# Performance work log

Hardware: AMD Instinct MI355X
Metric: run time of the kernel (lower is better)

The kernel has to match this reference:

```python
import jax, jax.numpy as jnp
import numpy as np


def setup_inputs() -> dict:
    key = jax.random.key(0)
    kq, kk, kv = jax.random.split(key, 3)
    d_head, sq, skv = 128, 8192, 8192
    q = jax.random.normal(kq, (d_head, sq), dtype=jnp.float32)
    k = jax.random.normal(kk, (d_head, skv), dtype=jnp.float32)
    v = jax.random.normal(kv, (d_head, skv), dtype=jnp.float32)
    return {"q": q, "k": k, "v": v}


def reference(q, k, v):
    # qk: (seqlen_q, seqlen_kv) -- full score matrix, no 1/sqrt(d) scaling (faithful)
    qk = jnp.einsum('dq,dk->qk', q, k)
    row_max = jnp.max(qk, axis=1, keepdims=True)
    exp_row = jnp.exp(qk - row_max)
    scores = exp_row / jnp.sum(exp_row, axis=1, keepdims=True)
    # attn_out: (seqlen_q, d_head)
    attn_out = jnp.einsum('qk,dk->qd', scores, v)
    return attn_out
```

## Files before the change

kernel.cpp:

```cpp
#include <hip/hip_runtime.h>
#include <hip/hip_bf16.h>
#include <math.h>

typedef _Float16 half8 __attribute__((ext_vector_type(8)));
typedef __fp16 fp16x2 __attribute__((ext_vector_type(2)));
typedef float f32x4 __attribute__((ext_vector_type(4)));
typedef float f32x16 __attribute__((ext_vector_type(16)));

#define D 128
#define SQ 8192
#define SKV 8192
#define BQ 256
#define BKV 64
#define LOG2E 1.4426950408889634f
#define DEFER_THR 11.5417f

__device__ __forceinline__ float bf2f(ushort h) {
  union { unsigned u; float f; } v; v.u = ((unsigned)h) << 16;
  return v.f;
}
__device__ __forceinline__ unsigned cvtpk_bf(float a, float b) {
  unsigned r;
  asm("v_cvt_pk_bf16_f32 %0, %1, %2" : "=v"(r) : "v"(a), "v"(b));
  return r;
}
__device__ __forceinline__ unsigned cvtpk_h(float a, float b) {
  union { fp16x2 h; unsigned u; } r;
  r.h = __builtin_amdgcn_cvt_pkrtz(a, b);
  return r.u;
}
__device__ __forceinline__ float fexp2(float x) {
  float r;
  asm("v_exp_f32 %0, %1" : "=v"(r) : "v"(x));
  return r;
}
__device__ __forceinline__ void pl32swap(unsigned& a, unsigned& b) {
  asm("v_permlane32_swap_b32 %0, %1" : "+v"(a), "+v"(b));
}

__global__ void prep_all(const float* __restrict__ q, const float* __restrict__ k,
                         const float* __restrict__ v,
                         _Float16* __restrict__ QT, _Float16* __restrict__ PK,
                         _Float16* __restrict__ PV) {
  int b = blockIdx.x;
  int t = threadIdx.x;
  if (b < 512) {
    const bool isQ = (b < 256);
    const float* src = isQ ? q : k;
    const float scl = isQ ? LOG2E : 1.0f;
    int s0 = (isQ ? b : b - 256) * 32;
    __shared__ float lds[128][33];
    int dr = t >> 5, l = t & 31;
#pragma unroll
    for (int j = 0; j < 16; ++j) {
      int dd = dr * 16 + j;
      lds[dd][l] = src[(size_t)dd * SQ + s0 + l];
    }
    __syncthreads();
#pragma unroll
    for (int i = 0; i < 2; ++i) {
      int cid = t + i * 256;
      int c = cid >> 5, sl = cid & 31;
      half8 hv;
#pragma unroll
      for (int e = 0; e < 8; ++e) hv[e] = (_Float16)(lds[c * 8 + e][sl] * scl);
      if (isQ) {
        *(half8*)(QT + (size_t)(s0 + sl) * D + c * 8) = hv;
      } else {
        int srow = s0 + sl;
        size_t elem = (size_t)((srow >> 5) * 8 + (c >> 1)) * 512 +
                      ((c & 1) * 32 + (srow & 31)) * 8;
        *(half8*)(PK + elem) = hv;
      }
    }
  } else {
    int idx = (b - 512) * 256 + t;
    int i8 = idx * 8;
    float4 x0 = *(const float4*)(v + i8);
    float4 x1 = *(const float4*)(v + i8 + 4);
    int drow = i8 >> 13;
    int kv = i8 & (SKV - 1);
    size_t elem = (size_t)(kv >> 6) * 8192 +
                  (size_t)((drow >> 5) * 4 + ((kv >> 4) & 3)) * 512 +
                  (((kv >> 3) & 1) * 32 + (drow & 31)) * 8;
    half8 hv = { (_Float16)x0.x, (_Float16)x0.y, (_Float16)x0.z, (_Float16)x0.w,
                 (_Float16)x1.x, (_Float16)x1.y, (_Float16)x1.z, (_Float16)x1.w };
    *(half8*)(PV + elem) = hv;
  }
}

__global__ __launch_bounds__(512, 2)
void flash_fwd(const _Float16* __restrict__ QT, const _Float16* __restrict__ PK,
               const _Float16* __restrict__ PV,
               ushort* __restrict__ Opart, float* __restrict__ Mst,
               float* __restrict__ Lst, int splitLen) {
  __shared__ _Float16 Kl[2][BKV * D];
  __shared__ _Float16 Vl[3][BKV * D];

  const int tid = threadIdx.x;
  const int w = tid >> 6;
  const int lane = tid & 63;
  const int lc = lane & 31;
  const int hi = lane >> 5;
  const int qb = blockIdx.x;
  const int split = blockIdx.y;
  const int qrow = qb * BQ + w * 32 + lc;

  half8 qh[8];
#pragma unroll
  for (int ds = 0; ds < 8; ++ds)
    qh[ds] = *(const half8*)(QT + (size_t)qrow * D + ds * 16 + hi * 8);

  f32x16 Ot[4];
#pragma unroll
  for (int dt = 0; dt < 4; ++dt)
#pragma unroll
    for (int e = 0; e < 16; ++e) Ot[dt][e] = 0.f;
  float mrun = -INFINITY, lrun = 0.f;

  const int kvBase = split * splitLen;
  const int nsteps = splitLen / BKV;
  const int tB = kvBase / BKV;

#define STAGE(KB, VB, T)                                                      \
  {                                                                           \
    _Pragma("unroll")                                                         \
    for (int j = 0; j < 4; ++j) {                                             \
      int cblk = w * 4 + j;                                                   \
      int cc = cblk & 15;                                                     \
      const _Float16* gp = ((cblk < 16) ? PK : PV) +                          \
                           (size_t)(T) * (BKV * D) + cc * 512 + lane * 8;     \
      _Float16* lp = ((cblk < 16) ? &Kl[KB][0] : &Vl[VB][0]) + cc * 512;      \
      __builtin_amdgcn_global_load_lds(                                       \
          (const __attribute__((address_space(1))) unsigned*)gp,              \
          (__attribute__((address_space(3))) unsigned*)lp, 16, 0, 0);         \
    }                                                                         \
  }

  auto QKX = [&](int kb2, f32x16& s0, f32x16& s1) {
    const _Float16* kb = &Kl[kb2][0] + lane * 8;
#pragma unroll
    for (int e = 0; e < 16; ++e) { s0[e] = 0.f; s1[e] = 0.f; }
    __builtin_amdgcn_s_setprio(1);
#pragma unroll
    for (int ds = 0; ds < 8; ++ds) {
      half8 k0 = *(const half8*)(kb + ds * 512);
      half8 k1 = *(const half8*)(kb + (8 + ds) * 512);
      s0 = __builtin_amdgcn_mfma_f32_32x32x16_f16(k0, qh[ds], s0, 0, 0, 0);
      s1 = __builtin_amdgcn_mfma_f32_32x32x16_f16(k1, qh[ds], s1, 0, 0, 0);
    }
    __builtin_amdgcn_s_setprio(0);
  };

  auto SMPV = [&](f32x16& s0, f32x16& s1, int vb3) {
    float t8[8];
#pragma unroll
    for (int e = 0; e < 8; ++e)
      t8[e] = fmaxf(fmaxf(s0[e], s0[e + 8]), fmaxf(s1[e], s1[e + 8]));
    float mx = fmaxf(fmaxf(fmaxf(t8[0], t8[4]), fmaxf(t8[1], t8[5])),
                     fmaxf(fmaxf(t8[2], t8[6]), fmaxf(t8[3], t8[7])));
    mx = fmaxf(mx, __shfl_xor(mx, 32));
    if (!__all(mx - mrun <= DEFER_THR)) {
      float mn = fmaxf(mrun, mx);
      float sc = fexp2(mrun - mn);
      mrun = mn;
      lrun *= sc;
#pragma unroll
      for (int dt = 0; dt < 4; ++dt)
#pragma unroll
        for (int e = 0; e < 16; ++e) Ot[dt][e] *= sc;
    }
#pragma unroll
    for (int e = 0; e < 16; ++e) {
      s0[e] = fexp2(s0[e] - mrun);
      s1[e] = fexp2(s1[e] - mrun);
    }
    float a8[8];
#pragma unroll
    for (int e = 0; e < 8; ++e) a8[e] = (s0[e] + s0[e + 8]) + (s1[e] + s1[e + 8]);
    float lsum = ((a8[0] + a8[4]) + (a8[1] + a8[5])) +
                 ((a8[2] + a8[6]) + (a8[3] + a8[7]));
    lsum += __shfl_xor(lsum, 32);
    lrun += lsum;

    unsigned pk[8];
    half8 pb[4];
    union { unsigned u[4]; half8 v; } pbu;
#pragma unroll
    for (int j = 0; j < 8; ++j) pk[j] = cvtpk_h(s0[2 * j], s0[2 * j + 1]);
    pl32swap(pk[0], pk[2]); pl32swap(pk[1], pk[3]);
    pl32swap(pk[4], pk[6]); pl32swap(pk[5], pk[7]);
    pbu.u[0] = pk[0]; pbu.u[1] = pk[1]; pbu.u[2] = pk[2]; pbu.u[3] = pk[3]; pb[0] = pbu.v;
    pbu.u[0] = pk[4]; pbu.u[1] = pk[5]; pbu.u[2] = pk[6]; pbu.u[3] = pk[7]; pb[1] = pbu.v;
#pragma unroll
    for (int j = 0; j < 8; ++j) pk[j] = cvtpk_h(s1[2 * j], s1[2 * j + 1]);
    pl32swap(pk[0], pk[2]); pl32swap(pk[1], pk[3]);
    pl32swap(pk[4], pk[6]); pl32swap(pk[5], pk[7]);
    pbu.u[0] = pk[0]; pbu.u[1] = pk[1]; pbu.u[2] = pk[2]; pbu.u[3] = pk[3]; pb[2] = pbu.v;
    pbu.u[0] = pk[4]; pbu.u[1] = pk[5]; pbu.u[2] = pk[6]; pbu.u[3] = pk[7]; pb[3] = pbu.v;

    const _Float16* vb = &Vl[vb3][0] + lane * 8;
    __builtin_amdgcn_s_setprio(1);
#pragma unroll
    for (int dt = 0; dt < 4; ++dt) {
      half8 v0 = *(const half8*)(vb + (dt * 4 + 0) * 512);
      half8 v1 = *(const half8*)(vb + (dt * 4 + 1) * 512);
      half8 v2 = *(const half8*)(vb + (dt * 4 + 2) * 512);
      half8 v3 = *(const half8*)(vb + (dt * 4 + 3) * 512);
      Ot[dt] = __builtin_amdgcn_mfma_f32_32x32x16_f16(v0, pb[0], Ot[dt], 0, 0, 0);
      Ot[dt] = __builtin_amdgcn_mfma_f32_32x32x16_f16(v1, pb[1], Ot[dt], 0, 0, 0);
      Ot[dt] = __builtin_amdgcn_mfma_f32_32x32x16_f16(v2, pb[2], Ot[dt], 0, 0, 0);
      Ot[dt] = __builtin_amdgcn_mfma_f32_32x32x16_f16(v3, pb[3], Ot[dt], 0, 0, 0);
    }
    __builtin_amdgcn_s_setprio(0);
  };

  f32x16 sA0, sA1, sB0, sB1;

  STAGE(0, 0, tB);
  __syncthreads();
  if (nsteps > 1) STAGE(1, 1, tB + 1);
  QKX(0, sA0, sA1);
  __syncthreads();

  int p = 1;
  for (; p + 1 < nsteps; p += 2) {
    STAGE(0, (p + 1) % 3, tB + p + 1);
    QKX(1, sB0, sB1);
    SMPV(sA0, sA1, (p - 1) % 3);
    __syncthreads();
    if (p + 2 < nsteps) STAGE(1, (p + 2) % 3, tB + p + 2);
    QKX(0, sA0, sA1);
    SMPV(sB0, sB1, p % 3);
    __syncthreads();
  }
  if (p < nsteps) {
    QKX(1, sB0, sB1);
    SMPV(sA0, sA1, (p - 1) % 3);
    SMPV(sB0, sB1, p % 3);
  } else {
    SMPV(sA0, sA1, (nsteps - 1) % 3);
  }

  ushort* Op = Opart + (size_t)split * SQ * D + (size_t)qrow * D;
#pragma unroll
  for (int dt = 0; dt < 4; ++dt) {
#pragma unroll
    for (int rg = 0; rg < 4; ++rg) {
      uint2 o2;
      o2.x = cvtpk_bf(Ot[dt][4 * rg + 0], Ot[dt][4 * rg + 1]);
      o2.y = cvtpk_bf(Ot[dt][4 * rg + 2], Ot[dt][4 * rg + 3]);
      *(uint2*)(Op + dt * 32 + rg * 8 + hi * 4) = o2;
    }
  }
  if (hi == 0) {
    Mst[split * SQ + qrow] = mrun;
    Lst[split * SQ + qrow] = lrun;
  }
}

__global__ void combine(const ushort* __restrict__ Opart, const float* __restrict__ Mst,
                        const float* __restrict__ Lst, float* __restrict__ out, int nsplit) {
  int t4 = (blockIdx.x * 256 + threadIdx.x) * 4;
  int qi = t4 >> 7;
  float M = -INFINITY;
  for (int s = 0; s < nsplit; ++s) M = fmaxf(M, Mst[s * SQ + qi]);
  float n0 = 0.f, n1 = 0.f, n2 = 0.f, n3 = 0.f, den = 0.f;
  for (int s = 0; s < nsplit; ++s) {
    float wgt = fexp2(Mst[s * SQ + qi] - M);
    den += wgt * Lst[s * SQ + qi];
    ushort4 u = *(const ushort4*)(Opart + (size_t)s * SQ * D + t4);
    n0 += wgt * bf2f(u.x); n1 += wgt * bf2f(u.y);
    n2 += wgt * bf2f(u.z); n3 += wgt * bf2f(u.w);
  }
  float inv = 1.0f / den;
  float4 o = { n0 * inv, n1 * inv, n2 * inv, n3 * inv };
  *(float4*)(out + t4) = o;
}

extern "C" void kernel_launch(void* const* d_in, const int* in_sizes, int n_in,
                              void* d_out, int out_size, void* d_ws, size_t ws_size,
                              hipStream_t stream) {
  const float* q = (const float*)d_in[0];
  const float* k = (const float*)d_in[1];
  const float* v = (const float*)d_in[2];
  float* out = (float*)d_out;

  char* ws = (char*)d_ws;
  const size_t mat = (size_t)SQ * D * 2;
  _Float16* QT = (_Float16*)(ws);
  _Float16* PK = (_Float16*)(ws + mat);
  _Float16* PV = (_Float16*)(ws + 2 * mat);
  char* rest = ws + 3 * mat;

  const size_t opartSz = (size_t)SQ * D * 2;
  const size_t statSz  = (size_t)SQ * 4;
  int nsplit = 8;
  while (nsplit > 1 &&
         3 * mat + (size_t)nsplit * (opartSz + 2 * statSz) > ws_size) nsplit >>= 1;

  ushort* Opart = (ushort*)rest;
  float* Mst = (float*)(rest + (size_t)nsplit * opartSz);
  float* Lst = (float*)(rest + (size_t)nsplit * opartSz + (size_t)nsplit * statSz);

  prep_all<<<1024, 256, 0, stream>>>(q, k, v, QT, PK, PV);
  flash_fwd<<<dim3(SQ / BQ, nsplit), 512, 0, stream>>>(QT, PK, PV,
                                                       Opart, Mst, Lst, SKV / nsplit);
  combine<<<(SQ * D) / (256 * 4), 256, 0, stream>>>(Opart, Mst, Lst, out, nsplit);
}
```

Baseline: 58.51 us.

## Deepen LDS ring to prefetch two KV tiles ahead with one barrier per pair

Grows the shared-memory K ring to four buffers and the V ring to five, then restructures the main loop. Each iteration prefetches the tiles two steps ahead, runs both QK products, then both softmax/PV passes, with a single barrier per pair of steps. The aim is to hide global-to-LDS latency and cut barrier count. The cost is LDS use rising to about 144KB per block, which likely allows only one block per CU despite launch bounds asking for two. The loop also silently assumes an even step count.

Measured after the change: 60.10 us. 1.03x slower.

```diff
diff --git a/kernel.cpp b/kernel.cpp
--- a/kernel.cpp
+++ b/kernel.cpp
@@ -94,8 +94,8 @@
                const _Float16* __restrict__ PV,
                ushort* __restrict__ Opart, float* __restrict__ Mst,
                float* __restrict__ Lst, int splitLen) {
-  __shared__ _Float16 Kl[2][BKV * D];
-  __shared__ _Float16 Vl[3][BKV * D];
+  __shared__ _Float16 Kl[4][BKV * D];
+  __shared__ _Float16 Vl[5][BKV * D];
 
   const int tid = threadIdx.x;
   const int w = tid >> 6;
@@ -137,8 +137,8 @@
     }                                                                         \
   }
 
-  auto QKX = [&](int kb2, f32x16& s0, f32x16& s1) {
-    const _Float16* kb = &Kl[kb2][0] + lane * 8;
+  auto QKX = [&](int kb4, f32x16& s0, f32x16& s1) {
+    const _Float16* kb = &Kl[kb4][0] + lane * 8;
 #pragma unroll
     for (int e = 0; e < 16; ++e) { s0[e] = 0.f; s1[e] = 0.f; }
     __builtin_amdgcn_s_setprio(1);
@@ -152,7 +152,7 @@
     __builtin_amdgcn_s_setprio(0);
   };
 
-  auto SMPV = [&](f32x16& s0, f32x16& s1, int vb3) {
+  auto SMPV = [&](f32x16& s0, f32x16& s1, int vb5) {
     float t8[8];
 #pragma unroll
     for (int e = 0; e < 8; ++e)
@@ -199,7 +199,7 @@
     pbu.u[0] = pk[0]; pbu.u[1] = pk[1]; pbu.u[2] = pk[2]; pbu.u[3] = pk[3]; pb[2] = pbu.v;
     pbu.u[0] = pk[4]; pbu.u[1] = pk[5]; pbu.u[2] = pk[6]; pbu.u[3] = pk[7]; pb[3] = pbu.v;
 
-    const _Float16* vb = &Vl[vb3][0] + lane * 8;
+    const _Float16* vb = &Vl[vb5][0] + lane * 8;
     __builtin_amdgcn_s_setprio(1);
 #pragma unroll
     for (int dt = 0; dt < 4; ++dt) {
@@ -215,31 +215,20 @@
     __builtin_amdgcn_s_setprio(0);
   };
 
+  STAGE(0, 0, tB + 0);
+  STAGE(1, 1, tB + 1);
+  __syncthreads();
+
   f32x16 sA0, sA1, sB0, sB1;
-
-  STAGE(0, 0, tB);
-  __syncthreads();
-  if (nsteps > 1) STAGE(1, 1, tB + 1);
-  QKX(0, sA0, sA1);
-  __syncthreads();
-
-  int p = 1;
-  for (; p + 1 < nsteps; p += 2) {
-    STAGE(0, (p + 1) % 3, tB + p + 1);
-    QKX(1, sB0, sB1);
-    SMPV(sA0, sA1, (p - 1) % 3);
+  for (int s = 0; s < nsteps / 2; ++s) {
+    const int a = 2 * s, b = a + 1;
+    if (a + 2 < nsteps) STAGE((a + 2) & 3, (a + 2) % 5, tB + a + 2);
+    if (b + 2 < nsteps) STAGE((b + 2) & 3, (b + 2) % 5, tB + b + 2);
+    QKX(a & 3, sA0, sA1);
+    QKX(b & 3, sB0, sB1);
+    SMPV(sA0, sA1, a % 5);
+    SMPV(sB0, sB1, b % 5);
     __syncthreads();
-    if (p + 2 < nsteps) STAGE(1, (p + 2) % 3, tB + p + 2);
-    QKX(0, sA0, sA1);
-    SMPV(sB0, sB1, p % 3);
-    __syncthreads();
-  }
-  if (p < nsteps) {
-    QKX(1, sB0, sB1);
-    SMPV(sA0, sA1, (p - 1) % 3);
-    SMPV(sB0, sB1, p % 3);
-  } else {
-    SMPV(sA0, sA1, (nsteps - 1) % 3);
   }
 
   ushort* Op = Opart + (size_t)split * SQ * D + (size_t)qrow * D;
```
